# Optimization experiments

Measured on AMD Instinct MI355X. Metric: run time of the kernel, lower is better.

Reference implementation:

```python
import jax, jax.numpy as jnp
import numpy as np

N = 100000
E = 600000
IN_DIM = 256
H0 = 128
H1 = 64
EPS = 1e-5


def setup_inputs() -> dict:
    key = jax.random.key(0)
    ks = jax.random.split(key, 12)
    x = jax.random.normal(ks[0], (N, IN_DIM), dtype=jnp.float32)
    edge_index = jax.random.randint(ks[1], (2, E), 0, N, dtype=jnp.int64)
    edge_weight = jax.random.uniform(ks[2], (E,), dtype=jnp.float32)
    def lin(k, fan_in, fan_out):
        bound = 1.0 / np.sqrt(fan_in)
        k1, k2 = jax.random.split(k)
        W = jax.random.uniform(k1, (fan_in, fan_out), minval=-bound, maxval=bound, dtype=jnp.float32)
        b = jax.random.uniform(k2, (fan_out,), minval=-bound, maxval=bound, dtype=jnp.float32)
        return W, b
    W0, b0 = lin(ks[3], IN_DIM, H0)
    W1, b1 = lin(ks[4], H0, H0)
    W2, b2 = lin(ks[5], H0, H0)
    pW, pb = lin(ks[6], H0, H1)
    return {
        'x': x, 'edge_index': edge_index, 'edge_weight': edge_weight,
        'bn_gamma': jnp.ones((IN_DIM,), jnp.float32), 'bn_beta': jnp.zeros((IN_DIM,), jnp.float32),
        'W0': W0, 'b0': b0, 'W1': W1, 'b1': b1, 'W2': W2, 'b2': b2,
        'pbn_gamma': jnp.ones((H0,), jnp.float32), 'pbn_beta': jnp.zeros((H0,), jnp.float32),
        'pW': pW, 'pb': pb,
    }


def batchnorm(x, gamma, beta):
    # BatchNorm1d training-mode forward: per-feature batch statistics over nodes
    mean = jnp.mean(x, axis=0)
    var = jnp.mean(jnp.square(x - mean), axis=0)  # biased var, as torch BN forward
    return (x - mean) * jax.lax.rsqrt(var + EPS) * gamma + beta


def gcn_conv(x, src, dst, norm, W, b):
    # PyG GCNConv (add_self_loops=False): transform then normalized aggregation
    h = x @ W                                   # [N, out]
    msg = norm[:, None] * h[src]                # gather + scale, [E, out]
    out = jax.ops.segment_sum(msg, dst, num_segments=N)  # scatter-add
    return out + b


def reference(x, edge_index, edge_weight, bn_gamma, bn_beta, W0, b0, W1, b1, W2, b2, pbn_gamma, pbn_beta, pW, pb):
    src, dst = edge_index[0], edge_index[1]
    # gcn_norm without self loops: D^-1/2 A D^-1/2
    deg = jax.ops.segment_sum(edge_weight, dst, num_segments=N)
    dis = jnp.where(deg > 0, jax.lax.rsqrt(jnp.maximum(deg, EPS)), 0.0)
    norm = dis[src] * edge_weight * dis[dst]    # [E]

    h = batchnorm(x, bn_gamma, bn_beta)
    h = jax.nn.relu(gcn_conv(h, src, dst, norm, W0, b0))
    h = jax.nn.relu(gcn_conv(h, src, dst, norm, W1, b1))
    h = jax.nn.relu(gcn_conv(h, src, dst, norm, W2, b2))
    # project head: BN -> Linear -> ReLU
    h = batchnorm(h, pbn_gamma, pbn_beta)
    h = jax.nn.relu(h @ pW + pb)
    return h
```

## Files before the change

### kernel.cpp

```cpp
#include <hip/hip_runtime.h>


constexpr int NN    = 100000;
constexpr int NEDGE = 600000;
constexpr int INDIM = 256;
constexpr int HD    = 128;
constexpr int OUTD  = 64;
constexpr int EB    = (NEDGE + 255) / 256;
constexpr int SB    = 1024;
constexpr int NB    = (NN + 255) / 256;
constexpr int WB    = 257;
constexpr int GG    = (NN + 127) / 128;
constexpr int A2B   = 1024;
#define EPSV 1e-5f

typedef __bf16 bf16x8 __attribute__((ext_vector_type(8)));
typedef float  f32x4  __attribute__((ext_vector_type(4)));

__device__ __forceinline__ float bf2f(unsigned short u) {
    unsigned int v = ((unsigned int)u) << 16;
    return __builtin_bit_cast(float, v);
}
__device__ __forceinline__ unsigned short f2bf(float f) {
    __bf16 h = (__bf16)f;
    return __builtin_bit_cast(unsigned short, h);
}
__device__ __forceinline__ unsigned int pk2(float a, float b) {
    return (unsigned int)f2bf(a) | ((unsigned int)f2bf(b) << 16);
}
__device__ __forceinline__ void atomAdd(float* p, float v) {
    unsafeAtomicAdd(p, v);
}

template <int K, int M, bool RELU_OUT, bool OUT_BF16, bool A_F32>
__device__ __forceinline__ void mgemm_body(int bid, int tid, char* smem,
                                           const void* __restrict__ Araw,
                                           const unsigned short* __restrict__ Bt,
                                           const float* __restrict__ outBias,
                                           void* __restrict__ Craw, int n) {
    constexpr int BK  = 64;
    constexpr int LDA = BK + 8;
    unsigned short* As = (unsigned short*)smem;
    unsigned short* Bs = As + 128 * LDA;

    const int wave = tid >> 6, lane = tid & 63;
    const int quad = lane >> 4, mrow = lane & 15;
    const int row0 = bid * 128;

    constexpr int RT = (M == 128) ? 4 : 2;
    constexpr int CT = 4;
    const int rowbase = (M == 128) ? ((wave >> 1) * 64) : (wave * 32);
    const int colbase = (M == 128) ? ((wave & 1) * 64) : 0;

    f32x4 acc[RT][CT];
#pragma unroll
    for (int i = 0; i < RT; i++)
#pragma unroll
        for (int j = 0; j < CT; j++) acc[i][j] = (f32x4){0.f, 0.f, 0.f, 0.f};

    for (int k0 = 0; k0 < K; k0 += BK) {
        if (k0) __syncthreads();
#pragma unroll
        for (int p = 0; p < 4; p++) {
            int c   = p * 256 + tid;
            int r   = c >> 3;
            int c8  = (c & 7) * 8;
            int grow = row0 + r;
            uint4 u = make_uint4(0, 0, 0, 0);
            if (grow < n) {
                if constexpr (A_F32) {
                    const float* Af = (const float*)Araw;
                    float4 fa = *(const float4*)&Af[(size_t)grow * K + k0 + c8];
                    float4 fb = *(const float4*)&Af[(size_t)grow * K + k0 + c8 + 4];
                    u.x = pk2(fa.x, fa.y); u.y = pk2(fa.z, fa.w);
                    u.z = pk2(fb.x, fb.y); u.w = pk2(fb.z, fb.w);
                } else {
                    const unsigned short* Ab = (const unsigned short*)Araw;
                    u = *(const uint4*)&Ab[(size_t)grow * K + k0 + c8];
                }
            }
            *(uint4*)&As[r * LDA + c8] = u;
        }
#pragma unroll
        for (int p = 0; p < M / 32; p++) {
            int c  = p * 256 + tid;
            int r  = c >> 3;
            int c8 = (c & 7) * 8;
            *(uint4*)&Bs[r * LDA + c8] = *(const uint4*)&Bt[(size_t)r * K + k0 + c8];
        }
        __syncthreads();

#pragma unroll
        for (int ks = 0; ks < BK; ks += 32) {
            bf16x8 af[RT], bfr[CT];
#pragma unroll
            for (int i = 0; i < RT; i++)
                af[i] = *(const bf16x8*)&As[(rowbase + i * 16 + mrow) * LDA + ks + quad * 8];
#pragma unroll
            for (int j = 0; j < CT; j++)
                bfr[j] = *(const bf16x8*)&Bs[(colbase + j * 16 + mrow) * LDA + ks + quad * 8];
#pragma unroll
            for (int i = 0; i < RT; i++)
#pragma unroll
                for (int j = 0; j < CT; j++)
                    acc[i][j] = __builtin_amdgcn_mfma_f32_16x16x32_bf16(
                        af[i], bfr[j], acc[i][j], 0, 0, 0);
        }
    }

#pragma unroll
    for (int i = 0; i < RT; i++) {
#pragma unroll
        for (int r = 0; r < 4; r++) {
            int row = row0 + rowbase + i * 16 + quad * 4 + r;
            if (row < n) {
#pragma unroll
                for (int j = 0; j < CT; j++) {
                    int col = colbase + j * 16 + mrow;
                    float v = acc[i][j][r];
                    if (outBias) v += outBias[col];
                    if (RELU_OUT) v = fmaxf(v, 0.f);
                    if (OUT_BF16)
                        ((unsigned short*)Craw)[(size_t)row * M + col] = f2bf(v);
                    else
                        ((float*)Craw)[(size_t)row * M + col] = v;
                }
            }
        }
    }
}

template <bool L1>
__device__ __forceinline__ void gather8(const unsigned short* __restrict__ tg,
                                        uint2* __restrict__ edata,
                                        const float* __restrict__ dis,
                                        float id, int gl,
                                        int i, int beg, int end, float* acc) {
    uint4 v[8]; float w[8]; uint2 ed[8];
#pragma unroll
    for (int k = 0; k < 8; k++) {
        int  idx = i + k;
        bool ok  = idx < end;
        ed[k] = edata[ok ? idx : beg];
    }
#pragma unroll
    for (int k = 0; k < 8; k++) {
        bool ok = (i + k) < end;
        float wt = __builtin_bit_cast(float, ed[k].y);
        if (L1) wt = dis[ed[k].x] * wt * id;
        w[k] = ok ? wt : 0.f;
        v[k] = *(const uint4*)&tg[(size_t)ed[k].x * HD];
    }
    if (L1) {
#pragma unroll
        for (int k = 0; k < 8; k++)
            if (gl == 0 && (i + k) < end)
                edata[i + k].y = __builtin_bit_cast(unsigned, w[k]);
    }
#pragma unroll
    for (int k = 0; k < 8; k++) {
        acc[0] += w[k] * bf2f((unsigned short)(v[k].x & 0xffff));
        acc[1] += w[k] * bf2f((unsigned short)(v[k].x >> 16));
        acc[2] += w[k] * bf2f((unsigned short)(v[k].y & 0xffff));
        acc[3] += w[k] * bf2f((unsigned short)(v[k].y >> 16));
        acc[4] += w[k] * bf2f((unsigned short)(v[k].z & 0xffff));
        acc[5] += w[k] * bf2f((unsigned short)(v[k].z >> 16));
        acc[6] += w[k] * bf2f((unsigned short)(v[k].w & 0xffff));
        acc[7] += w[k] * bf2f((unsigned short)(v[k].w >> 16));
    }
}

template <bool L1>
__global__ __launch_bounds__(256) void fagg_gemm_k(const unsigned short* __restrict__ t,
                                                   const int* __restrict__ rowptr,
                                                   uint2* __restrict__ edata,
                                                   const float* __restrict__ dis,
                                                   const float* __restrict__ bias,
                                                   const unsigned short* __restrict__ Bt,
                                                   unsigned short* __restrict__ Cout,
                                                   int n) {
    constexpr int LDAa = HD + 8;
    constexpr int LDAb = 64 + 8;
    __shared__ unsigned short As[128 * LDAa];
    __shared__ unsigned short Bs[HD * LDAb];

    const int tid  = threadIdx.x;
    const int row0 = blockIdx.x * 128;

    {
        const int g  = tid >> 4;
        const int gl = tid & 15;
        const unsigned short* tg = t + gl * 8;
        float4 bb0 = *(const float4*)&bias[gl * 8];
        float4 bb1 = *(const float4*)&bias[gl * 8 + 4];
        for (int rr = 0; rr < 8; rr++) {
            int node = row0 + g * 8 + rr;
            float acc[8];
#pragma unroll
            for (int j = 0; j < 8; j++) acc[j] = 0.f;
            if (node < n) {
                int beg = rowptr[node], end = rowptr[node + 1];
                float id = L1 ? dis[node] : 0.f;
                for (int i = beg; i < end; i += 8)
                    gather8<L1>(tg, edata, dis, id, gl, i, beg, end, acc);
            }
            float r0 = fmaxf(acc[0] + bb0.x, 0.f), r1 = fmaxf(acc[1] + bb0.y, 0.f);
            float r2 = fmaxf(acc[2] + bb0.z, 0.f), r3 = fmaxf(acc[3] + bb0.w, 0.f);
            float r4 = fmaxf(acc[4] + bb1.x, 0.f), r5 = fmaxf(acc[5] + bb1.y, 0.f);
            float r6 = fmaxf(acc[6] + bb1.z, 0.f), r7 = fmaxf(acc[7] + bb1.w, 0.f);
            uint4 o;
            o.x = pk2(r0, r1);
            o.y = pk2(r2, r3);
            o.z = pk2(r4, r5);
            o.w = pk2(r6, r7);
            *(uint4*)&As[(g * 8 + rr) * LDAa + gl * 8] = o;
        }
    }

    const int wave = tid >> 6, lane = tid & 63;
    const int quad = lane >> 4, mrow = lane & 15;
    const int rowbase = (wave >> 1) * 64;
    const int colbase = (wave & 1) * 64;

    f32x4 acc[4][4];
#pragma unroll
    for (int i = 0; i < 4; i++)
#pragma unroll
        for (int j = 0; j < 4; j++) acc[i][j] = (f32x4){0.f, 0.f, 0.f, 0.f};

    for (int k0 = 0; k0 < HD; k0 += 64) {
        if (k0) __syncthreads();
#pragma unroll
        for (int p = 0; p < 4; p++) {
            int c  = p * 256 + tid;
            int r  = c >> 3;
            int c8 = (c & 7) * 8;
            *(uint4*)&Bs[r * LDAb + c8] = *(const uint4*)&Bt[(size_t)r * HD + k0 + c8];
        }
        __syncthreads();
#pragma unroll
        for (int ks = 0; ks < 64; ks += 32) {
            bf16x8 af[4], bfr[4];
#pragma unroll
            for (int i = 0; i < 4; i++)
                af[i] = *(const bf16x8*)&As[(rowbase + i * 16 + mrow) * LDAa + k0 + ks + quad * 8];
#pragma unroll
            for (int j = 0; j < 4; j++)
                bfr[j] = *(const bf16x8*)&Bs[(colbase + j * 16 + mrow) * LDAb + ks + quad * 8];
#pragma unroll
            for (int i = 0; i < 4; i++)
#pragma unroll
                for (int j = 0; j < 4; j++)
                    acc[i][j] = __builtin_amdgcn_mfma_f32_16x16x32_bf16(
                        af[i], bfr[j], acc[i][j], 0, 0, 0);
        }
    }

#pragma unroll
    for (int i = 0; i < 4; i++) {
#pragma unroll
        for (int r = 0; r < 4; r++) {
            int row = row0 + rowbase + i * 16 + quad * 4 + r;
            if (row < n) {
#pragma unroll
                for (int j = 0; j < 4; j++) {
                    int col = colbase + j * 16 + mrow;
                    Cout[(size_t)row * HD + col] = f2bf(acc[i][j][r]);
                }
            }
        }
    }
}

__global__ __launch_bounds__(256) void front_k(const int* __restrict__ dst,
                                               int* __restrict__ cnt,
                                               int* __restrict__ rank,
                                               const float* __restrict__ x,
                                               float* __restrict__ sums) {
    __shared__ float red[256 * 8];
    const int tid = threadIdx.x;
    const int bx  = blockIdx.x;
    if ((bx & 1) == 0) {
        for (int i = (bx >> 1) * 256 + tid; i < NEDGE; i += 1024 * 256) {
            int d = dst[i];
            rank[i] = atomicAdd(&cnt[d], 1);
        }
        return;
    }
    const int bid = bx >> 1;
    const int cg  = tid & 63;
    const int rs  = tid >> 6;
    float s0 = 0.f, s1 = 0.f, s2 = 0.f, s3 = 0.f;
    float q0 = 0.f, q1 = 0.f, q2 = 0.f, q3 = 0.f;
    for (int r0 = bid * 16; r0 < NN; r0 += SB * 16) {
        float4 v[4];
#pragma unroll
        for (int j = 0; j < 4; j++)
            v[j] = *(const float4*)&x[(size_t)(r0 + rs + j * 4) * INDIM + cg * 4];
#pragma unroll
        for (int j = 0; j < 4; j++) {
            s0 += v[j].x; s1 += v[j].y; s2 += v[j].z; s3 += v[j].w;
            q0 += v[j].x * v[j].x; q1 += v[j].y * v[j].y;
            q2 += v[j].z * v[j].z; q3 += v[j].w * v[j].w;
        }
    }
    red[tid * 8 + 0] = s0; red[tid * 8 + 1] = s1;
    red[tid * 8 + 2] = s2; red[tid * 8 + 3] = s3;
    red[tid * 8 + 4] = q0; red[tid * 8 + 5] = q1;
    red[tid * 8 + 6] = q2; red[tid * 8 + 7] = q3;
    __syncthreads();
    int cgr = tid >> 2, j = tid & 3;
    float a = 0.f, b = 0.f;
#pragma unroll
    for (int r2 = 0; r2 < 4; r2++) {
        a += red[(r2 * 64 + cgr) * 8 + j];
        b += red[(r2 * 64 + cgr) * 8 + 4 + j];
    }
    atomAdd(&sums[tid], a);
    atomAdd(&sums[INDIM + tid], b);
}

__global__ __launch_bounds__(256) void mid_k(const int* __restrict__ cnt,
                                             int* __restrict__ rowptr,
                                             int* __restrict__ bsum,
                                             const float* __restrict__ stats,
                                             const float* __restrict__ gamma,
                                             const float* __restrict__ beta,
                                             const float* __restrict__ W0,
                                             const float* __restrict__ W1,
                                             const float* __restrict__ W2,
                                             unsigned short* __restrict__ W0t,
                                             unsigned short* __restrict__ W1t,
                                             unsigned short* __restrict__ W2t,
                                             float* __restrict__ d0, float invN) {
    __shared__ float sm[512];
    const int tid = threadIdx.x;
    if (blockIdx.x < NB) {
        int* s = (int*)sm;
        int i = blockIdx.x * 256 + tid;
        s[tid] = (i < NN) ? cnt[i] : 0;
        __syncthreads();
        for (int d = 1; d < 256; d <<= 1) {
            int t = (tid >= d) ? s[tid - d] : 0;
            __syncthreads();
            s[tid] += t;
            __syncthreads();
        }
        if (i < NN) rowptr[i + 1] = s[tid];
        if (tid == 255) bsum[blockIdx.x] = s[255];
        return;
    }
    const int b = blockIdx.x - NB;
    float* sA = sm;
    float* sC = sm + 256;
    {
        float mean = stats[tid] * invN;
        float var  = stats[INDIM + tid] * invN - mean * mean;
        float a    = gamma[tid] * rsqrtf(var + EPSV);
        sA[tid] = a;
        sC[tid] = beta[tid] - mean * a;
    }
    __syncthreads();
    if (b < 128) {
        int i = b * 256 + tid, k = i >> 7, j = i & 127;
        W0t[(size_t)j * INDIM + k] = f2bf(W0[i] * sA[k]);
    } else if (b < 192) {
        int i = (b - 128) * 256 + tid, k = i >> 7, j = i & 127;
        W1t[(size_t)j * HD + k] = f2bf(W1[i]);
    } else if (b < 256) {
        int i = (b - 192) * 256 + tid, k = i >> 7, j = i & 127;
        W2t[(size_t)j * HD + k] = f2bf(W2[i]);
    } else {
        if (tid < HD) {
            float s = 0.f;
            for (int ff = 0; ff < INDIM; ff++) s += sC[ff] * W0[ff * HD + tid];
            d0[tid] = s;
        }
    }
}

__global__ __launch_bounds__(512) void scan2_k(int* __restrict__ bsum, int nb) {
    __shared__ int s[512];
    s[threadIdx.x] = (threadIdx.x < (unsigned)nb) ? bsum[threadIdx.x] : 0;
    __syncthreads();
    for (int d = 1; d < 512; d <<= 1) {
        int t = (threadIdx.x >= d) ? s[threadIdx.x - d] : 0;
        __syncthreads();
        s[threadIdx.x] += t;
        __syncthreads();
    }
    if (threadIdx.x < (unsigned)nb) bsum[threadIdx.x] = s[threadIdx.x];
}

__global__ __launch_bounds__(256) void scan3_k(int* __restrict__ rowptr,
                                               const int* __restrict__ bsum, int n) {
    int i = blockIdx.x * 256 + threadIdx.x;
    if (i == 0) rowptr[0] = 0;
    if (i < n) {
        int v = rowptr[i + 1];
        if (blockIdx.x > 0) v += bsum[blockIdx.x - 1];
        rowptr[i + 1] = v;
    }
}

__global__ __launch_bounds__(256) void sg0_k(const int* __restrict__ src,
                                             const int* __restrict__ dst,
                                             const float* __restrict__ ew,
                                             const int* __restrict__ rank,
                                             const int* __restrict__ rowptr,
                                             uint2* __restrict__ edata,
                                             const float* __restrict__ x,
                                             const unsigned short* __restrict__ W0t,
                                             const float* __restrict__ d0,
                                             unsigned short* __restrict__ tbufA) {
    __shared__ char smem[(128 * 72 + 128 * 72) * 2];
    if (blockIdx.x < EB) {
        int i = blockIdx.x * 256 + threadIdx.x;
        if (i < NEDGE) {
            int s = src[i], d = dst[i];
            int p = rowptr[d] + rank[i];
            edata[p] = make_uint2((unsigned)s, __builtin_bit_cast(unsigned, ew[i]));
        }
        return;
    }
    mgemm_body<INDIM, HD, false, true, true>(blockIdx.x - EB, threadIdx.x, smem,
                                             x, W0t, d0, tbufA, NN);
}

__global__ __launch_bounds__(256) void degnorm_k(const int* __restrict__ rowptr,
                                                 const uint2* __restrict__ edata,
                                                 float* __restrict__ dis) {
    int n = blockIdx.x * 256 + threadIdx.x;
    if (n < NN) {
        int beg = rowptr[n], end = rowptr[n + 1];
        float s = 0.f;
        for (int j = beg; j < end; j++)
            s += __builtin_bit_cast(float, edata[j].y);
        dis[n] = (s > 0.f) ? rsqrtf(fmaxf(s, EPSV)) : 0.f;
    }
}

__global__ __launch_bounds__(256) void agg2_stats_k(const unsigned short* __restrict__ t,
                                                    const int* __restrict__ rowptr,
                                                    uint2* __restrict__ edata,
                                                    const float* __restrict__ bias,
                                                    unsigned short* __restrict__ agg,
                                                    float* __restrict__ sums, int n) {
    const int tid = threadIdx.x, g = tid >> 4, gl = tid & 15;
    const unsigned short* tg = t + gl * 8;
    float4 bb0 = *(const float4*)&bias[gl * 8];
    float4 bb1 = *(const float4*)&bias[gl * 8 + 4];
    float ssum[8], ssq[8];
#pragma unroll
    for (int j = 0; j < 8; j++) { ssum[j] = 0.f; ssq[j] = 0.f; }

    for (int node0 = blockIdx.x * 16; node0 < n; node0 += A2B * 16) {
        int node = node0 + g;
        float acc[8];
#pragma unroll
        for (int j = 0; j < 8; j++) acc[j] = 0.f;
        if (node < n) {
            int beg = rowptr[node], end = rowptr[node + 1];
            for (int i = beg; i < end; i += 8)
                gather8<false>(tg, edata, nullptr, 0.f, gl, i, beg, end, acc);
        }
        float r[8];
        r[0] = fmaxf(acc[0] + bb0.x, 0.f); r[1] = fmaxf(acc[1] + bb0.y, 0.f);
        r[2] = fmaxf(acc[2] + bb0.z, 0.f); r[3] = fmaxf(acc[3] + bb0.w, 0.f);
        r[4] = fmaxf(acc[4] + bb1.x, 0.f); r[5] = fmaxf(acc[5] + bb1.y, 0.f);
        r[6] = fmaxf(acc[6] + bb1.z, 0.f); r[7] = fmaxf(acc[7] + bb1.w, 0.f);
        if (node < n) {
            uint4 o;
            o.x = pk2(r[0], r[1]);
            o.y = pk2(r[2], r[3]);
            o.z = pk2(r[4], r[5]);
            o.w = pk2(r[6], r[7]);
            *(uint4*)&agg[(size_t)node * HD + gl * 8] = o;
#pragma unroll
            for (int j = 0; j < 8; j++) { ssum[j] += r[j]; ssq[j] += r[j] * r[j]; }
        }
    }

    __shared__ float red[256 * 16];
#pragma unroll
    for (int j = 0; j < 8; j++) {
        red[tid * 16 + j]     = ssum[j];
        red[tid * 16 + 8 + j] = ssq[j];
    }
    __syncthreads();
    if (tid < HD) {
        int glr = tid >> 3, j = tid & 7;
        float a = 0.f, b = 0.f;
#pragma unroll
        for (int g2 = 0; g2 < 16; g2++) {
            a += red[(g2 * 16 + glr) * 16 + j];
            b += red[(g2 * 16 + glr) * 16 + 8 + j];
        }
        atomAdd(&sums[tid], a);
        atomAdd(&sums[HD + tid], b);
    }
}

__global__ __launch_bounds__(256) void wprep2_k(const float* __restrict__ stats2,
                                                const float* __restrict__ gamma,
                                                const float* __restrict__ beta,
                                                const float* __restrict__ pW,
                                                const float* __restrict__ pb,
                                                unsigned short* __restrict__ pWt,
                                                float* __restrict__ dfin, float invN) {
    __shared__ float sA[HD], sC[HD];
    int f = threadIdx.x;
    if (f < HD) {
        float mean = stats2[f] * invN;
        float var  = stats2[HD + f] * invN - mean * mean;
        float a    = gamma[f] * rsqrtf(var + EPSV);
        sA[f] = a;
        sC[f] = beta[f] - mean * a;
    }
    __syncthreads();
    int b = blockIdx.x, tid = threadIdx.x;
    if (b < 32) {
        int i = b * 256 + tid, k = i >> 6, j = i & 63;
        pWt[(size_t)j * HD + k] = f2bf(pW[i] * sA[k]);
    } else {
        if (tid < OUTD) {
            float s = pb[tid];
            for (int ff = 0; ff < HD; ff++) s += sC[ff] * pW[ff * OUTD + tid];
            dfin[tid] = s;
        }
    }
}

__global__ __launch_bounds__(256) void gemm3_k(const unsigned short* __restrict__ A,
                                               const unsigned short* __restrict__ Bt,
                                               const float* __restrict__ outBias,
                                               float* __restrict__ C, int n) {
    __shared__ char smem[(128 * 72 + OUTD * 72) * 2];
    mgemm_body<HD, OUTD, true, false, false>(blockIdx.x, threadIdx.x, smem,
                                             A, Bt, outBias, C, n);
}

extern "C" void kernel_launch(void* const* d_in, const int* in_sizes, int n_in,
                              void* d_out, int out_size, void* d_ws, size_t ws_size,
                              hipStream_t stream) {
    const float* x        = (const float*)d_in[0];
    const int*   ei       = (const int*)d_in[1];
    const float* ew       = (const float*)d_in[2];
    const float* bn_gamma = (const float*)d_in[3];
    const float* bn_beta  = (const float*)d_in[4];
    const float* W0       = (const float*)d_in[5];
    const float* b0       = (const float*)d_in[6];
    const float* W1       = (const float*)d_in[7];
    const float* b1       = (const float*)d_in[8];
    const float* W2       = (const float*)d_in[9];
    const float* b2       = (const float*)d_in[10];
    const float* pgamma   = (const float*)d_in[11];
    const float* pbeta    = (const float*)d_in[12];
    const float* pW       = (const float*)d_in[13];
    const float* pb       = (const float*)d_in[14];
    float* out = (float*)d_out;

    const int* srcp = ei;
    const int* dstp = ei + NEDGE;

    char*  base = (char*)d_ws;
    size_t off  = 0;
    auto carve = [&](size_t bytes) -> void* {
        void* p = (void*)(base + off);
        off = (off + bytes + 255) & ~(size_t)255;
        return p;
    };
    int*            cnt    = (int*)carve(NN * 4);
    float*          stats  = (float*)carve(2 * INDIM * 4);
    float*          stats2 = (float*)carve(2 * HD * 4);
    int*            rowptr = (int*)carve((NN + 1) * 4);
    int*            rank   = (int*)carve((size_t)NEDGE * 4);
    float*          dis    = (float*)carve(NN * 4);
    int*            bsum   = (int*)carve(512 * 4);
    uint2*          edata  = (uint2*)carve((size_t)NEDGE * 8);
    float*          d0     = (float*)carve(HD * 4);
    float*          dfin   = (float*)carve(OUTD * 4);
    unsigned short* W0t    = (unsigned short*)carve((size_t)INDIM * HD * 2);
    unsigned short* W1t    = (unsigned short*)carve((size_t)HD * HD * 2);
    unsigned short* W2t    = (unsigned short*)carve((size_t)HD * HD * 2);
    unsigned short* pWt    = (unsigned short*)carve((size_t)HD * OUTD * 2);
    unsigned short* tbufA  = (unsigned short*)carve((size_t)NN * HD * 2);
    unsigned short* tbufB  = (unsigned short*)carve((size_t)NN * HD * 2);
    unsigned short* aggb   = (unsigned short*)carve((size_t)NN * HD * 2);
    (void)ws_size;

    hipMemsetAsync(cnt, 0, (size_t)((char*)stats2 - (char*)cnt) + 2 * HD * 4, stream);

    front_k<<<2048, 256, 0, stream>>>(dstp, cnt, rank, x, stats);

    mid_k<<<NB + WB, 256, 0, stream>>>(cnt, rowptr, bsum, stats, bn_gamma, bn_beta,
                                       W0, W1, W2, W0t, W1t, W2t, d0, 1.f / NN);
    scan2_k<<<1, 512, 0, stream>>>(bsum, NB);
    scan3_k<<<NB, 256, 0, stream>>>(rowptr, bsum, NN);

    sg0_k<<<EB + GG, 256, 0, stream>>>(srcp, dstp, ew, rank, rowptr, edata,
                                       x, W0t, d0, tbufA);

    degnorm_k<<<NB, 256, 0, stream>>>(rowptr, edata, dis);

    fagg_gemm_k<true><<<GG, 256, 0, stream>>>(tbufA, rowptr, edata, dis, b0, W1t, tbufB, NN);
    fagg_gemm_k<false><<<GG, 256, 0, stream>>>(tbufB, rowptr, edata, dis, b1, W2t, tbufA, NN);

    agg2_stats_k<<<A2B, 256, 0, stream>>>(tbufA, rowptr, edata, b2, aggb, stats2, NN);

    wprep2_k<<<33, 256, 0, stream>>>(stats2, pgamma, pbeta, pW, pb, pWt, dfin,
                                     1.f / NN);
    gemm3_k<<<GG, 256, 0, stream>>>(aggb, pWt, dfin, out, NN);

    (void)n_in; (void)in_sizes; (void)out_size;
}
```

Before: 436.2 us.

## Stage block edge list in LDS, swizzle A tile, read weights directly from global

The fused aggregate+GEMM kernel now copies each block's contiguous edge range into shared memory once and gathers from it, with a global fallback when the range exceeds capacity. Row pointers are loaded once per lane and distributed by shuffle. The A tile uses an XOR-swizzled unpadded layout, and the B operand is read straight from global memory instead of being staged through LDS, which removes the K-loop barriers. Launch bounds request 4 blocks per CU. The cost is extra syncs and an LDS copy up front, plus uncoalesced global reads for B that rely on caching.

```diff
diff --git a/kernel.cpp b/kernel.cpp
--- a/kernel.cpp
+++ b/kernel.cpp
@@ -132,7 +132,8 @@
 
 template <bool L1>
 __device__ __forceinline__ void gather8(const unsigned short* __restrict__ tg,
-                                        uint2* __restrict__ edata,
+                                        const uint2* __restrict__ rde,
+                                        uint2* __restrict__ we,
                                         const float* __restrict__ dis,
                                         float id, int gl,
                                         int i, int beg, int end, float* acc) {
@@ -141,7 +142,7 @@
     for (int k = 0; k < 8; k++) {
         int  idx = i + k;
         bool ok  = idx < end;
-        ed[k] = edata[ok ? idx : beg];
+        ed[k] = rde[ok ? idx : beg];
     }
 #pragma unroll
     for (int k = 0; k < 8; k++) {
@@ -155,7 +156,7 @@
 #pragma unroll
         for (int k = 0; k < 8; k++)
             if (gl == 0 && (i + k) < end)
-                edata[i + k].y = __builtin_bit_cast(unsigned, w[k]);
+                we[i + k].y = __builtin_bit_cast(unsigned, w[k]);
     }
 #pragma unroll
     for (int k = 0; k < 8; k++) {
@@ -171,38 +172,60 @@
 }
 
 template <bool L1>
-__global__ __launch_bounds__(256) void fagg_gemm_k(const unsigned short* __restrict__ t,
-                                                   const int* __restrict__ rowptr,
-                                                   uint2* __restrict__ edata,
-                                                   const float* __restrict__ dis,
-                                                   const float* __restrict__ bias,
-                                                   const unsigned short* __restrict__ Bt,
-                                                   unsigned short* __restrict__ Cout,
-                                                   int n) {
-    constexpr int LDAa = HD + 8;
-    constexpr int LDAb = 64 + 8;
-    __shared__ unsigned short As[128 * LDAa];
-    __shared__ unsigned short Bs[HD * LDAb];
+__global__ __launch_bounds__(256, 4) void fagg_gemm_k(const unsigned short* __restrict__ t,
+                                                      const int* __restrict__ rowptr,
+                                                      uint2* __restrict__ edata,
+                                                      const float* __restrict__ dis,
+                                                      const float* __restrict__ bias,
+                                                      const unsigned short* __restrict__ Bt,
+                                                      unsigned short* __restrict__ Cout,
+                                                      int n) {
+    constexpr int MAXE = 1016;
+    __shared__ unsigned short As[128 * 128];
+    __shared__ uint2 ebuf[MAXE];
+    __shared__ int sbe[2];
 
     const int tid  = threadIdx.x;
     const int row0 = blockIdx.x * 128;
+    const int nblk = min(128, n - row0);
+
+    if (tid == 0) { sbe[0] = rowptr[row0]; sbe[1] = rowptr[row0 + nblk]; }
+    __syncthreads();
+    const int beg0 = sbe[0];
+    const int esz  = sbe[1] - beg0;
+    const bool fits = (esz <= MAXE);
+    if (fits)
+        for (int i = tid; i < esz; i += 256) ebuf[i] = edata[beg0 + i];
+    __syncthreads();
 
     {
         const int g  = tid >> 4;
         const int gl = tid & 15;
+        const int lanebase = (g & 3) * 16;
         const unsigned short* tg = t + gl * 8;
         float4 bb0 = *(const float4*)&bias[gl * 8];
         float4 bb1 = *(const float4*)&bias[gl * 8 + 4];
+        int ridx = row0 + g * 8 + ((gl < 9) ? gl : 8);
+        if (ridx > n) ridx = n;
+        int rp = rowptr[ridx];
+
         for (int rr = 0; rr < 8; rr++) {
             int node = row0 + g * 8 + rr;
             float acc[8];
 #pragma unroll
             for (int j = 0; j < 8; j++) acc[j] = 0.f;
             if (node < n) {
-                int beg = rowptr[node], end = rowptr[node + 1];
+                int beg = __shfl(rp, lanebase + rr, 64);
+                int end = __shfl(rp, lanebase + rr + 1, 64);
                 float id = L1 ? dis[node] : 0.f;
-                for (int i = beg; i < end; i += 8)
-                    gather8<L1>(tg, edata, dis, id, gl, i, beg, end, acc);
+                if (fits) {
+                    const uint2* rde = (const uint2*)ebuf - beg0;
+                    for (int i = beg; i < end; i += 8)
+                        gather8<L1>(tg, rde, edata, dis, id, gl, i, beg, end, acc);
+                } else {
+                    for (int i = beg; i < end; i += 8)
+                        gather8<L1>(tg, edata, edata, dis, id, gl, i, beg, end, acc);
+                }
             }
             float r0 = fmaxf(acc[0] + bb0.x, 0.f), r1 = fmaxf(acc[1] + bb0.y, 0.f);
             float r2 = fmaxf(acc[2] + bb0.z, 0.f), r3 = fmaxf(acc[3] + bb0.w, 0.f);
@@ -213,9 +236,12 @@
             o.y = pk2(r2, r3);
             o.z = pk2(r4, r5);
             o.w = pk2(r6, r7);
-            *(uint4*)&As[(g * 8 + rr) * LDAa + gl * 8] = o;
-        }
-    }
+            int row  = g * 8 + rr;
+            int bcol = (gl * 16) ^ ((row & 7) << 4);
+            *(uint4*)((char*)As + row * 256 + bcol) = o;
+        }
+    }
+    __syncthreads();
 
     const int wave = tid >> 6, lane = tid & 63;
     const int quad = lane >> 4, mrow = lane & 15;
@@ -228,32 +254,24 @@
 #pragma unroll
         for (int j = 0; j < 4; j++) acc[i][j] = (f32x4){0.f, 0.f, 0.f, 0.f};
 
-    for (int k0 = 0; k0 < HD; k0 += 64) {
-        if (k0) __syncthreads();
-#pragma unroll
-        for (int p = 0; p < 4; p++) {
-            int c  = p * 256 + tid;
-            int r  = c >> 3;
-            int c8 = (c & 7) * 8;
-            *(uint4*)&Bs[r * LDAb + c8] = *(const uint4*)&Bt[(size_t)r * HD + k0 + c8];
-        }
-        __syncthreads();
-#pragma unroll
-        for (int ks = 0; ks < 64; ks += 32) {
-            bf16x8 af[4], bfr[4];
-#pragma unroll
-            for (int i = 0; i < 4; i++)
-                af[i] = *(const bf16x8*)&As[(rowbase + i * 16 + mrow) * LDAa + k0 + ks + quad * 8];
+#pragma unroll 2
+    for (int k0 = 0; k0 < HD; k0 += 32) {
+        bf16x8 af[4], bfr[4];
+#pragma unroll
+        for (int i = 0; i < 4; i++) {
+            int row  = rowbase + i * 16 + mrow;
+            int bcol = ((k0 + quad * 8) * 2) ^ ((row & 7) << 4);
+            af[i] = *(const bf16x8*)((const char*)As + row * 256 + bcol);
+        }
+#pragma unroll
+        for (int j = 0; j < 4; j++)
+            bfr[j] = *(const bf16x8*)&Bt[(size_t)(colbase + j * 16 + mrow) * HD + k0 + quad * 8];
+#pragma unroll
+        for (int i = 0; i < 4; i++)
 #pragma unroll
             for (int j = 0; j < 4; j++)
-                bfr[j] = *(const bf16x8*)&Bs[(colbase + j * 16 + mrow) * LDAb + ks + quad * 8];
-#pragma unroll
-            for (int i = 0; i < 4; i++)
-#pragma unroll
-                for (int j = 0; j < 4; j++)
-                    acc[i][j] = __builtin_amdgcn_mfma_f32_16x16x32_bf16(
-                        af[i], bfr[j], acc[i][j], 0, 0, 0);
-        }
+                acc[i][j] = __builtin_amdgcn_mfma_f32_16x16x32_bf16(
+                    af[i], bfr[j], acc[i][j], 0, 0, 0);
     }
 
 #pragma unroll
@@ -462,7 +480,7 @@
         if (node < n) {
             int beg = rowptr[node], end = rowptr[node + 1];
             for (int i = beg; i < end; i += 8)
-                gather8<false>(tg, edata, nullptr, 0.f, gl, i, beg, end, acc);
+                gather8<false>(tg, edata, edata, nullptr, 0.f, gl, i, beg, end, acc);
         }
         float r[8];
         r[0] = fmaxf(acc[0] + bb0.x, 0.f); r[1] = fmaxf(acc[1] + bb0.y, 0.f);
```

After: 411.5 us. -5.7%, faster.
